# Kernel optimization log

Hardware: AMD Instinct MI355X
Metric: run time of the kernel (lower is better)

## Reference

```python
import jax, jax.numpy as jnp
import numpy as np


def setup_inputs() -> dict:
    key = jax.random.key(0)
    B, N, D = 4, 8192, 16
    inputs = jax.random.normal(key, (B, N, D), dtype=jnp.float32)
    return {"inputs": inputs, "k": 16}


def reference(inputs, k):
    # pairwise squared distances: ||x_i||^2 - 2 x_i.x_j + ||x_j||^2  -> [B, N, N]
    inner = -2.0 * jnp.einsum("bnd,bmd->bnm", inputs, inputs)
    square = jnp.sum(inputs * inputs, axis=-1, keepdims=True)  # [B, N, 1]
    adj = square + inner + jnp.swapaxes(square, 1, 2)          # [B, N, N]
    # k smallest distances -> top-k of negated matrix
    _, nn_idx = jax.lax.top_k(-adj, k)                          # [B, N, k]
    return nn_idx
```

## Files before the change

kernel.cpp:

```cpp
#include <hip/hip_runtime.h>


#define B_    4
#define N_    8192
#define D_    16
#define K_    16
#define SEGS_ 8
#define SEG_  (N_ / SEGS_)
#define CH_   8
#define NCH_  (SEG_ / CH_)
#define BT_   512
#define CAP_  10
#define NQ_   (B_ * N_)

typedef unsigned long long u64;

__device__ __forceinline__ float np_norm16(const float* __restrict__ p) {
#pragma clang fp contract(off)
  float m[16];
#pragma unroll
  for (int d = 0; d < 16; ++d) m[d] = p[d] * p[d];
  float r[8];
#pragma unroll
  for (int j = 0; j < 8; ++j) r[j] = m[j] + m[j + 8];
  float q[4];
#pragma unroll
  for (int j = 0; j < 4; ++j) q[j] = r[j] + r[j + 4];
  return (q[0] + q[2]) + (q[1] + q[3]);
}

__device__ __forceinline__ unsigned mono32(float f) {
  unsigned u = __float_as_uint(f);
  return u ^ ((unsigned)((int)u >> 31) | 0x80000000u);
}

__global__ __launch_bounds__(256) void knn_norms(const float* __restrict__ x,
                                                 float* __restrict__ nrm) {
  int q = blockIdx.x * 256 + threadIdx.x;
  float row[16];
  const float4* xv = (const float4*)(x + (size_t)q * D_);
  float4 a = xv[0], b = xv[1], c = xv[2], d = xv[3];
  row[0]=a.x; row[1]=a.y; row[2]=a.z; row[3]=a.w;
  row[4]=b.x; row[5]=b.y; row[6]=b.z; row[7]=b.w;
  row[8]=c.x; row[9]=c.y; row[10]=c.z; row[11]=c.w;
  row[12]=d.x; row[13]=d.y; row[14]=d.z; row[15]=d.w;
  nrm[q] = np_norm16(row);
}

__device__ __forceinline__ void insert16(float d, int j, float (&kd)[K_], int (&ki)[K_]) {
  float cd = d; int ci = j;
#pragma unroll
  for (int p = 0; p < K_; ++p) {
    bool gt = kd[p] > cd;
    float t0 = gt ? cd : kd[p];
    float t1 = gt ? kd[p] : cd;
    int   t2 = gt ? ci : ki[p];
    int   t3 = gt ? ki[p] : ci;
    kd[p] = t0; cd = t1; ki[p] = t2; ci = t3;
  }
}

__device__ __forceinline__ void flushbuf(u64* __restrict__ pbuf, int tid,
                                         int& count, float& thr,
                                         float (&kd)[K_], int (&ki)[K_]) {
#pragma unroll 1
  for (int s = 0; s < CAP_; ++s) {
    if (s < count) {
      u64 e = pbuf[(size_t)s * BT_ + tid];
      float d = __uint_as_float((unsigned)(e >> 32));
      if (d < thr) {
        int j = (int)(e & 0xffffu);
        insert16(d, j, kd, ki);
        thr = kd[K_ - 1];
      }
    }
  }
  count = 0;
}

__global__ __launch_bounds__(BT_, 2) void knn_fused(const float* __restrict__ x,
                                                    const float* __restrict__ nrm,
                                                    int* __restrict__ out) {
  __shared__ u64 smem[6208];
  float4* stageR = (float4*)smem;
  float*  stageN = (float*)(smem + 1024);
  u64*    pbuf   = smem + 1088;

  const int tid  = threadIdx.x;
  const int w    = tid >> 6;
  const int lane = tid & 63;
  const int q    = blockIdx.x * 64 + lane;
  const int bq   = (int)((blockIdx.x * 64u) >> 13);
  const int row0 = bq * N_ + w * SEG_;
  const float* __restrict__ cbase = x + (size_t)row0 * D_;
  const float* __restrict__ nbase = nrm + row0;

  float qa[D_];
  {
    const float4* qv = (const float4*)(x + (size_t)q * D_);
    float4 v0 = qv[0], v1 = qv[1], v2 = qv[2], v3 = qv[3];
    qa[0]=v0.x; qa[1]=v0.y; qa[2]=v0.z; qa[3]=v0.w;
    qa[4]=v1.x; qa[5]=v1.y; qa[6]=v1.z; qa[7]=v1.w;
    qa[8]=v2.x; qa[9]=v2.y; qa[10]=v2.z; qa[11]=v2.w;
    qa[12]=v3.x; qa[13]=v3.y; qa[14]=v3.z; qa[15]=v3.w;
  }
  const float ni = nrm[q];

  float kd[K_]; int ki[K_];
#pragma unroll
  for (int p = 0; p < K_; ++p) { kd[p] = 3.4e38f; ki[p] = 0; }
  float thr = 3.4e38f;
  int count = 0;

  {
    const float4* gs = (const float4*)cbase;
    if (lane < 32) stageR[(w * 2 + 0) * 32 + lane] = gs[lane];
    if (lane < CH_) stageN[(w * 2 + 0) * CH_ + lane] = nbase[lane];
  }

#pragma unroll 1
  for (int c = 0; c < NCH_; ++c) {
    const int b = c & 1;
    float4 p0; float pn = 0.f;
    const bool more = (c + 1 < NCH_);
    if (more) {
      const float4* gs = (const float4*)(cbase + (size_t)(c + 1) * CH_ * D_);
      if (lane < 32) p0 = gs[lane];
      if (lane < CH_) pn = nbase[(c + 1) * CH_ + lane];
    }

    const float4* rows = stageR + (w * 2 + b) * 32;
    const float*  nn   = stageN + (w * 2 + b) * CH_;

#pragma unroll 1
    for (int t = 0; t < CH_; t += 2) {
      float4 r00 = rows[t*4+0], r01 = rows[t*4+1], r02 = rows[t*4+2], r03 = rows[t*4+3];
      float4 r10 = rows[t*4+4], r11 = rows[t*4+5], r12 = rows[t*4+6], r13 = rows[t*4+7];
      float nj0 = nn[t], nj1 = nn[t + 1];

      float c0[16] = {r00.x,r00.y,r00.z,r00.w, r01.x,r01.y,r01.z,r01.w,
                      r02.x,r02.y,r02.z,r02.w, r03.x,r03.y,r03.z,r03.w};
      float c1[16] = {r10.x,r10.y,r10.z,r10.w, r11.x,r11.y,r11.z,r11.w,
                      r12.x,r12.y,r12.z,r12.w, r13.x,r13.y,r13.z,r13.w};

      float dot0 = 0.f, dot1 = 0.f;
#pragma unroll
      for (int d = 0; d < D_; ++d) {
        dot0 = __builtin_fmaf(qa[d], c0[d], dot0);
        dot1 = __builtin_fmaf(qa[d], c1[d], dot1);
      }
      float d0, d1;
      {
#pragma clang fp contract(off)
        float i0 = -2.0f * dot0;  float i1 = -2.0f * dot1;
        float u0 = ni + i0;       float u1 = ni + i1;
        d0 = u0 + nj0;            d1 = u1 + nj1;
      }

      if (d0 < thr) {
        pbuf[(size_t)count * BT_ + tid] =
            ((u64)__float_as_uint(d0) << 32) | (unsigned)(c * CH_ + t);
        ++count;
      }
      if (d1 < thr) {
        pbuf[(size_t)count * BT_ + tid] =
            ((u64)__float_as_uint(d1) << 32) | (unsigned)(c * CH_ + t + 1);
        ++count;
      }
      if (__any(count >= CAP_ - 1)) flushbuf(pbuf, tid, count, thr, kd, ki);
    }

    if (more) {
      if (lane < 32) stageR[(w * 2 + (b ^ 1)) * 32 + lane] = p0;
      if (lane < CH_) stageN[(w * 2 + (b ^ 1)) * CH_ + lane] = pn;
    }
  }
  flushbuf(pbuf, tid, count, thr, kd, ki);

  u64* mrg = smem + 1088;
  const int half = lane >> 5;
  const int lm   = lane & 31;

  __syncthreads();
#pragma unroll 1
  for (int h = 0; h < 2; ++h) {
    if (half == h) {
#pragma unroll
      for (int p = 0; p < K_; ++p) {
        mrg[((size_t)w * 16 + p) * 32 + lm] =
            ((u64)mono32(kd[p]) << 32) | (unsigned)(w * SEG_ + ki[p]);
      }
    }
    __syncthreads();

    if (tid < 256) {
      const int m  = tid >> 3;
      const int s  = tid & 7;
      const int qi = h * 32 + m;
      const int gq = blockIdx.x * 64 + qi;
      int ptr = 0;
#pragma unroll 1
      for (int r = 0; r < K_; ++r) {
        u64 hd = mrg[((size_t)s * 16 + ptr) * 32 + m];
        u64 mv = hd, o;
        o = __shfl_xor(mv, 1); mv = (o < mv) ? o : mv;
        o = __shfl_xor(mv, 2); mv = (o < mv) ? o : mv;
        o = __shfl_xor(mv, 4); mv = (o < mv) ? o : mv;
        if (hd == mv) ++ptr;
        if (s == 0) out[(size_t)gq * K_ + r] = (int)(mv & 0xffffu);
      }
    }
    __syncthreads();
  }
}

extern "C" void kernel_launch(void* const* d_in, const int* in_sizes, int n_in,
                              void* d_out, int out_size, void* d_ws, size_t ws_size,
                              hipStream_t stream) {
  const float* x = (const float*)d_in[0];
  float* nrm = (float*)d_ws;
  int* out = (int*)d_out;

  knn_norms<<<NQ_ / 256, 256, 0, stream>>>(x, nrm);
  knn_fused<<<NQ_ / 64, BT_, 0, stream>>>(x, nrm, out);
}
```

Baseline: 334.6 us.

## Use packed FP32 FMA with interleaved candidate-pair staging layout

Candidate rows in the per-wave shared staging buffer are now stored interleaved in pairs (row 2p and 2p+1 per dimension). This lets the dot products for two candidates be computed together with v_pk_fma_f32, halving the VALU instruction count of the distance loop. The distance epilogue also uses packed mul/add, the candidate buffer capacity is raised, and the shared memory footprint grows accordingly. The packed ops are inline asm, which limits compiler scheduling, and each lane now issues two scalar global loads where it previously issued one float4 load.

```diff
diff --git a/kernel.cpp b/kernel.cpp
--- a/kernel.cpp
+++ b/kernel.cpp
@@ -10,10 +10,27 @@
 #define CH_   8
 #define NCH_  (SEG_ / CH_)
 #define BT_   512
-#define CAP_  10
+#define CAP_  12
 #define NQ_   (B_ * N_)
 
 typedef unsigned long long u64;
+typedef float v2f __attribute__((ext_vector_type(2)));
+
+__device__ __forceinline__ v2f pk_fma(v2f a, v2f b, v2f c) {
+  v2f d;
+  asm("v_pk_fma_f32 %0, %1, %2, %3" : "=v"(d) : "v"(a), "v"(b), "v"(c));
+  return d;
+}
+__device__ __forceinline__ v2f pk_mul(v2f a, v2f b) {
+  v2f d;
+  asm("v_pk_mul_f32 %0, %1, %2" : "=v"(d) : "v"(a), "v"(b));
+  return d;
+}
+__device__ __forceinline__ v2f pk_add(v2f a, v2f b) {
+  v2f d;
+  asm("v_pk_add_f32 %0, %1, %2" : "=v"(d) : "v"(a), "v"(b));
+  return d;
+}
 
 __device__ __forceinline__ float np_norm16(const float* __restrict__ p) {
 #pragma clang fp contract(off)
@@ -66,7 +83,7 @@
 #pragma unroll 1
   for (int s = 0; s < CAP_; ++s) {
     if (s < count) {
-      u64 e = pbuf[(size_t)s * BT_ + tid];
+      u64 e = pbuf[s * BT_ + tid];
       float d = __uint_as_float((unsigned)(e >> 32));
       if (d < thr) {
         int j = (int)(e & 0xffffu);
@@ -81,8 +98,8 @@
 __global__ __launch_bounds__(BT_, 2) void knn_fused(const float* __restrict__ x,
                                                     const float* __restrict__ nrm,
                                                     int* __restrict__ out) {
-  __shared__ u64 smem[6208];
-  float4* stageR = (float4*)smem;
+  __shared__ u64 smem[7232];
+  v2f*    stageT = (v2f*)smem;
   float*  stageN = (float*)(smem + 1024);
   u64*    pbuf   = smem + 1088;
 
@@ -95,16 +112,21 @@
   const float* __restrict__ cbase = x + (size_t)row0 * D_;
   const float* __restrict__ nbase = nrm + row0;
 
-  float qa[D_];
+  const int p_ = lane >> 4;
+  const int d_ = lane & 15;
+
+  v2f qq[D_];
   {
     const float4* qv = (const float4*)(x + (size_t)q * D_);
     float4 v0 = qv[0], v1 = qv[1], v2 = qv[2], v3 = qv[3];
-    qa[0]=v0.x; qa[1]=v0.y; qa[2]=v0.z; qa[3]=v0.w;
-    qa[4]=v1.x; qa[5]=v1.y; qa[6]=v1.z; qa[7]=v1.w;
-    qa[8]=v2.x; qa[9]=v2.y; qa[10]=v2.z; qa[11]=v2.w;
-    qa[12]=v3.x; qa[13]=v3.y; qa[14]=v3.z; qa[15]=v3.w;
+    qq[0]=(v2f){v0.x,v0.x}; qq[1]=(v2f){v0.y,v0.y}; qq[2]=(v2f){v0.z,v0.z}; qq[3]=(v2f){v0.w,v0.w};
+    qq[4]=(v2f){v1.x,v1.x}; qq[5]=(v2f){v1.y,v1.y}; qq[6]=(v2f){v1.z,v1.z}; qq[7]=(v2f){v1.w,v1.w};
+    qq[8]=(v2f){v2.x,v2.x}; qq[9]=(v2f){v2.y,v2.y}; qq[10]=(v2f){v2.z,v2.z}; qq[11]=(v2f){v2.w,v2.w};
+    qq[12]=(v2f){v3.x,v3.x}; qq[13]=(v2f){v3.y,v3.y}; qq[14]=(v2f){v3.z,v3.z}; qq[15]=(v2f){v3.w,v3.w};
   }
   const float ni = nrm[q];
+  const v2f nip = (v2f){ni, ni};
+  const v2f m2  = (v2f){-2.0f, -2.0f};
 
   float kd[K_]; int ki[K_];
 #pragma unroll
@@ -113,65 +135,71 @@
   int count = 0;
 
   {
-    const float4* gs = (const float4*)cbase;
-    if (lane < 32) stageR[(w * 2 + 0) * 32 + lane] = gs[lane];
+    float g0 = cbase[(2 * p_) * D_ + d_];
+    float g1 = cbase[(2 * p_ + 1) * D_ + d_];
+    stageT[(w * 2 + 0) * 64 + p_ * 16 + d_] = (v2f){g0, g1};
     if (lane < CH_) stageN[(w * 2 + 0) * CH_ + lane] = nbase[lane];
   }
 
 #pragma unroll 1
   for (int c = 0; c < NCH_; ++c) {
     const int b = c & 1;
-    float4 p0; float pn = 0.f;
+    float pg0 = 0.f, pg1 = 0.f, pn = 0.f;
     const bool more = (c + 1 < NCH_);
     if (more) {
-      const float4* gs = (const float4*)(cbase + (size_t)(c + 1) * CH_ * D_);
-      if (lane < 32) p0 = gs[lane];
+      const float* cb = cbase + (size_t)(c + 1) * CH_ * D_;
+      pg0 = cb[(2 * p_) * D_ + d_];
+      pg1 = cb[(2 * p_ + 1) * D_ + d_];
       if (lane < CH_) pn = nbase[(c + 1) * CH_ + lane];
     }
 
-    const float4* rows = stageR + (w * 2 + b) * 32;
-    const float*  nn   = stageN + (w * 2 + b) * CH_;
-
-#pragma unroll 1
-    for (int t = 0; t < CH_; t += 2) {
-      float4 r00 = rows[t*4+0], r01 = rows[t*4+1], r02 = rows[t*4+2], r03 = rows[t*4+3];
-      float4 r10 = rows[t*4+4], r11 = rows[t*4+5], r12 = rows[t*4+6], r13 = rows[t*4+7];
-      float nj0 = nn[t], nj1 = nn[t + 1];
-
-      float c0[16] = {r00.x,r00.y,r00.z,r00.w, r01.x,r01.y,r01.z,r01.w,
-                      r02.x,r02.y,r02.z,r02.w, r03.x,r03.y,r03.z,r03.w};
-      float c1[16] = {r10.x,r10.y,r10.z,r10.w, r11.x,r11.y,r11.z,r11.w,
-                      r12.x,r12.y,r12.z,r12.w, r13.x,r13.y,r13.z,r13.w};
-
-      float dot0 = 0.f, dot1 = 0.f;
-#pragma unroll
-      for (int d = 0; d < D_; ++d) {
-        dot0 = __builtin_fmaf(qa[d], c0[d], dot0);
-        dot1 = __builtin_fmaf(qa[d], c1[d], dot1);
-      }
-      float d0, d1;
-      {
-#pragma clang fp contract(off)
-        float i0 = -2.0f * dot0;  float i1 = -2.0f * dot1;
-        float u0 = ni + i0;       float u1 = ni + i1;
-        d0 = u0 + nj0;            d1 = u1 + nj1;
-      }
+    const float4* tp = (const float4*)(stageT + (w * 2 + b) * 64);
+    const float*  nW = stageN + (w * 2 + b) * CH_;
+    const int j0 = c * CH_;
+
+#pragma unroll 1
+    for (int p = 0; p < 4; ++p) {
+      float4 f0 = tp[p*8+0], f1 = tp[p*8+1], f2 = tp[p*8+2], f3 = tp[p*8+3];
+      float4 f4 = tp[p*8+4], f5 = tp[p*8+5], f6 = tp[p*8+6], f7 = tp[p*8+7];
+
+      v2f acc = (v2f){0.f, 0.f};
+      acc = pk_fma(qq[0],  (v2f){f0.x, f0.y}, acc);
+      acc = pk_fma(qq[1],  (v2f){f0.z, f0.w}, acc);
+      acc = pk_fma(qq[2],  (v2f){f1.x, f1.y}, acc);
+      acc = pk_fma(qq[3],  (v2f){f1.z, f1.w}, acc);
+      acc = pk_fma(qq[4],  (v2f){f2.x, f2.y}, acc);
+      acc = pk_fma(qq[5],  (v2f){f2.z, f2.w}, acc);
+      acc = pk_fma(qq[6],  (v2f){f3.x, f3.y}, acc);
+      acc = pk_fma(qq[7],  (v2f){f3.z, f3.w}, acc);
+      acc = pk_fma(qq[8],  (v2f){f4.x, f4.y}, acc);
+      acc = pk_fma(qq[9],  (v2f){f4.z, f4.w}, acc);
+      acc = pk_fma(qq[10], (v2f){f5.x, f5.y}, acc);
+      acc = pk_fma(qq[11], (v2f){f5.z, f5.w}, acc);
+      acc = pk_fma(qq[12], (v2f){f6.x, f6.y}, acc);
+      acc = pk_fma(qq[13], (v2f){f6.z, f6.w}, acc);
+      acc = pk_fma(qq[14], (v2f){f7.x, f7.y}, acc);
+      acc = pk_fma(qq[15], (v2f){f7.z, f7.w}, acc);
+
+      v2f ii  = pk_mul(m2, acc);
+      v2f uu  = pk_add(nip, ii);
+      v2f njp = *(const v2f*)(nW + 2 * p);
+      v2f dd  = pk_add(uu, njp);
+      float d0 = dd.x, d1 = dd.y;
+      const int j = j0 + 2 * p;
 
       if (d0 < thr) {
-        pbuf[(size_t)count * BT_ + tid] =
-            ((u64)__float_as_uint(d0) << 32) | (unsigned)(c * CH_ + t);
+        pbuf[count * BT_ + tid] = ((u64)__float_as_uint(d0) << 32) | (unsigned)j;
         ++count;
       }
       if (d1 < thr) {
-        pbuf[(size_t)count * BT_ + tid] =
-            ((u64)__float_as_uint(d1) << 32) | (unsigned)(c * CH_ + t + 1);
+        pbuf[count * BT_ + tid] = ((u64)__float_as_uint(d1) << 32) | (unsigned)(j + 1);
         ++count;
       }
       if (__any(count >= CAP_ - 1)) flushbuf(pbuf, tid, count, thr, kd, ki);
     }
 
     if (more) {
-      if (lane < 32) stageR[(w * 2 + (b ^ 1)) * 32 + lane] = p0;
+      stageT[(w * 2 + (b ^ 1)) * 64 + p_ * 16 + d_] = (v2f){pg0, pg1};
       if (lane < CH_) stageN[(w * 2 + (b ^ 1)) * CH_ + lane] = pn;
     }
   }
```

Measured after the change: 333.9 us. About the same (-0.2%).
